# Kernel tuning notes

Measured on AMD Instinct MI355X. Metric: run time of the kernel, lower is better.

Reference implementation:

```python
import math
import jax, jax.numpy as jnp
import numpy as np

B, N1, N2 = 4, 1024, 768
DIM, H, DK = 1536, 8, 64
DV = DIM // H          # 192
NRPF = DIM // H        # 192, divisible by 6
ESM_CELL = 1280 + 256  # 1536
LN_EPS = 1e-5


def layer_norm(t, g, b):
    mu = jnp.mean(t, axis=-1, keepdims=True)
    var = jnp.mean(jnp.square(t - mu), axis=-1, keepdims=True)
    return (t - mu) * jax.lax.rsqrt(var + LN_EPS) * g + b


def positional_embed(n, feature_size):
    # Enformer-style relative positional features for distances -n+1..n-1
    distances = jnp.arange(-n + 1, n, dtype=jnp.float32)  # [2n-1]
    absd = jnp.abs(distances)[:, None]
    nb = feature_size // 6  # 3 basis fns x 2 (sym + signed)
    seq_len = float(n)
    # exponential
    max_range = math.log(seq_len) / math.log(2.0)
    half_life = 2.0 ** jnp.linspace(3.0, max_range, nb)
    f_exp = jnp.exp(-math.log(2.0) / half_life * absd)
    # central mask
    widths = 2.0 ** jnp.arange(1, nb + 1, dtype=jnp.float32) - 1.0
    f_cm = (widths[None, :] > absd).astype(jnp.float32)
    # gamma pdf
    stddev = seq_len / (2.0 * nb)
    start_mean = seq_len / nb
    mean = jnp.linspace(start_mean, seq_len, nb)
    conc = (mean / stddev) ** 2
    rate = mean / stddev ** 2
    log_p = jax.scipy.special.xlogy(conc - 1.0, absd) - rate * absd
    log_norm = jax.scipy.special.gammaln(conc) - conc * jnp.log(rate)
    prob = jnp.exp(log_p - log_norm) + 1e-8
    f_gam = prob / jnp.max(prob, axis=-1, keepdims=True)
    emb = jnp.concatenate([f_exp, f_cm, f_gam], axis=-1)
    return jnp.concatenate([emb, jnp.sign(distances)[:, None] * emb], axis=-1)  # [2n-1, feature_size]


def relative_shift(x):
    # x: [b, h, t1, 2n-1] -> [b, h, t1, n]
    b, h, t1, _ = x.shape
    x = jnp.pad(x, ((0, 0), (0, 0), (0, 0), (1, 0)))
    t2 = x.shape[-1]  # 2n
    x = x.reshape(b, h, t2, t1)[:, :, 1:, :].reshape(b, h, t1, t2 - 1)
    return x[..., : (t2 + 1) // 2]


def ffn(t, g, b, w1, b1, w2, b2):
    h = layer_norm(t, g, b)
    h = jax.nn.relu(h @ w1 + b1)
    return h @ w2 + b2


def setup_inputs() -> dict:
    key = jax.random.key(0)
    ks = jax.random.split(key, 20)
    s = 0.02
    d = {
        'x': jax.random.normal(ks[0], (B, N1, DIM), jnp.float32),
        'y0': jax.random.normal(ks[1], (B, N2, ESM_CELL), jnp.float32),
        'res_w': jax.random.normal(ks[2], (ESM_CELL, DIM)) * s,
        'lnx_g': jnp.ones((DIM,)), 'lnx_b': jnp.zeros((DIM,)),
        'lny_g': jnp.ones((DIM,)), 'lny_b': jnp.zeros((DIM,)),
        'wq': jax.random.normal(ks[3], (DIM, H * DK)) * s,
        'wk': jax.random.normal(ks[4], (DIM, H * DK)) * s,
        'wv1': jax.random.normal(ks[5], (DIM, H * DV)) * s,
        'wv2': jax.random.normal(ks[6], (DIM, H * DV)) * s,
        'wrel': jax.random.normal(ks[7], (NRPF, H * DK)) * s,
        'rel_pos_bias': jax.random.normal(ks[8], (1, H, 1, DK)),
        'wo1': jax.random.normal(ks[9], (H * DV, DIM)) * s, 'bo1': jnp.zeros((DIM,)),
        'wo2': jax.random.normal(ks[10], (H * DV, DIM)) * s, 'bo2': jnp.zeros((DIM,)),
        'fx_ln_g': jnp.ones((DIM,)), 'fx_ln_b': jnp.zeros((DIM,)),
        'fx_w1': jax.random.normal(ks[11], (DIM, 2 * DIM)) * s, 'fx_b1': jnp.zeros((2 * DIM,)),
        'fx_w2': jax.random.normal(ks[12], (2 * DIM, DIM)) * s, 'fx_b2': jnp.zeros((DIM,)),
        'fy_ln_g': jnp.ones((DIM,)), 'fy_ln_b': jnp.zeros((DIM,)),
        'fy_w1': jax.random.normal(ks[13], (DIM, 2 * DIM)) * s, 'fy_b1': jnp.zeros((2 * DIM,)),
        'fy_w2': jax.random.normal(ks[14], (2 * DIM, DIM)) * s, 'fy_b2': jnp.zeros((DIM,)),
    }
    return d


def reference(x, y0, res_w, lnx_g, lnx_b, lny_g, lny_b, wq, wk, wv1, wv2,
              wrel, rel_pos_bias, wo1, bo1, wo2, bo2,
              fx_ln_g, fx_ln_b, fx_w1, fx_b1, fx_w2, fx_b2,
              fy_ln_g, fy_ln_b, fy_w1, fy_b1, fy_w2, fy_b2):
    scale = DK ** -0.5
    y = y0 @ res_w                                   # res_proj (first layer)
    x1 = layer_norm(x, lnx_g, lnx_b)
    y1 = layer_norm(y, lny_g, lny_b)

    def heads(t, dh):  # [b, n, h*dh] -> [b, h, n, dh]
        return t.reshape(t.shape[0], t.shape[1], H, dh).transpose(0, 2, 1, 3)

    q = heads(x1 @ wq, DK) * scale                   # [b,h,n1,dk]
    k = heads(y1 @ wk, DK)                           # [b,h,n2,dk]
    v2 = heads(y1 @ wv2, DV)                         # [b,h,n2,dv]

    content = jnp.einsum('bhid,bhjd->bhij', q, k)    # [b,h,n1,n2]

    pos = positional_embed(N1, NRPF)                 # [2n1-1, nrpf]
    rel_q = (pos @ wrel).reshape(2 * N1 - 1, H, DK).transpose(1, 0, 2)  # [h,2n1-1,dk]
    rel_logits = jnp.einsum('bhjd,hnd->bhjn', k * scale + rel_pos_bias, rel_q)  # [b,h,n2,2n1-1]
    rel_logits = relative_shift(rel_logits)          # [b,h,n2,n1]
    logits = content + rel_logits.transpose(0, 1, 3, 2)

    attn = jax.nn.softmax(logits, axis=-1)           # [b,h,n1,n2]

    out1 = jnp.einsum('bhij,bhjd->bhid', attn, v2)   # [b,h,n1,dv]
    out1 = out1.transpose(0, 2, 1, 3).reshape(B, N1, H * DV)
    x2 = out1 @ wo1 + bo1

    # exchange branch: reuse attn^T on v1 from stream x
    v1 = heads(x1 @ wv1, DV)                         # [b,h,n1,dv]
    out2 = jnp.einsum('bhij,bhid->bhjd', attn, v1)   # [b,h,n2,dv]
    out2 = out2.transpose(0, 2, 1, 3).reshape(B, N2, H * DV)
    y2 = out2 @ wo2 + bo2

    x4 = x + x2
    x5 = x4 + ffn(x4, fx_ln_g, fx_ln_b, fx_w1, fx_b1, fx_w2, fx_b2)
    y4 = y + y2
    y5 = y4 + ffn(y4, fy_ln_g, fy_ln_b, fy_w1, fy_b1, fy_w2, fy_b2)
    return x5, y5
```

## Files before the change

### kernel.cpp

```cpp
#include <hip/hip_runtime.h>
#include <stdint.h>
#include <math.h>

typedef __attribute__((ext_vector_type(8))) short s8v;
typedef __attribute__((ext_vector_type(4))) short s4v;
typedef __attribute__((ext_vector_type(4))) float f4v;

#define DEV static __device__ __forceinline__

DEV short f2bf(float f) {
  uint32_t u = __builtin_bit_cast(uint32_t, f);
  u += 0x7FFFu + ((u >> 16) & 1u);
  return (short)(u >> 16);
}
DEV float bf2f(short s) {
  uint32_t u = ((uint32_t)(uint16_t)s) << 16;
  return __builtin_bit_cast(float, u);
}

#define GLD16(g, l) __builtin_amdgcn_global_load_lds( \
    (const __attribute__((address_space(1))) void*)(g), \
    (__attribute__((address_space(3))) void*)(l), 16, 0, 0)

__global__ __launch_bounds__(256) void gemm_bt(
    const short* __restrict__ A, const short* __restrict__ B,
    float* Cf, short* Cb,
    const float* __restrict__ bias, const float* resid,
    int M, int N, int K, int lda, int ldb, int ldc,
    long long sAo, long long sAi, long long sBo, long long sBi,
    long long sCo, long long sCi, float alpha, int relu)
{
  __shared__ __align__(16) short lA[128*32];
  __shared__ __align__(16) short lB[128*32];
  const int z = blockIdx.z, zo = z >> 3, zi = z & 7;
  const short* Ab = A + zo*sAo + zi*sAi;
  const short* Bb = B + zo*sBo + zi*sBi;
  const long long cOff = zo*sCo + zi*sCi;

  const int m0 = blockIdx.y*128, n0 = blockIdx.x*128;
  const int tid = threadIdx.x, lane = tid & 63, wv = tid >> 6;
  const int wm = (wv >> 1)*64, wn = (wv & 1)*64;
  const int fr = lane & 15, fq = lane >> 4;

  f4v acc[4][4] = {};

  const int rA0 = min(m0 + (tid >> 2), M - 1);
  const int rA1 = min(m0 + 64 + (tid >> 2), M - 1);
  const int rB0 = min(n0 + (tid >> 2), N - 1);
  const int rB1 = min(n0 + 64 + (tid >> 2), N - 1);
  const int pc = (tid & 3) * 8;
  const short* gA0 = Ab + (size_t)rA0*lda + pc;
  const short* gA1 = Ab + (size_t)rA1*lda + pc;
  const short* gB0 = Bb + (size_t)rB0*ldb + pc;
  const short* gB1 = Bb + (size_t)rB1*ldb + pc;
  short* dA0 = lA + (wv*64)*8;
  short* dA1 = lA + (256 + wv*64)*8;
  short* dB0 = lB + (wv*64)*8;
  short* dB1 = lB + (256 + wv*64)*8;

  for (int k0 = 0; k0 < K; k0 += 32) {
    GLD16(gA0 + k0, dA0);
    GLD16(gA1 + k0, dA1);
    GLD16(gB0 + k0, dB0);
    GLD16(gB1 + k0, dB1);
    __syncthreads();
    s8v af[4], bg[4];
#pragma unroll
    for (int i = 0; i < 4; i++) {
      af[i] = *(const s8v*)&lA[(wm + i*16 + fr)*32 + fq*8];
      bg[i] = *(const s8v*)&lB[(wn + i*16 + fr)*32 + fq*8];
    }
#pragma unroll
    for (int mi = 0; mi < 4; mi++)
#pragma unroll
      for (int ni = 0; ni < 4; ni++)
        acc[mi][ni] = __builtin_amdgcn_mfma_f32_16x16x32_bf16(af[mi], bg[ni], acc[mi][ni], 0, 0, 0);
    __syncthreads();
  }

#pragma unroll
  for (int mi = 0; mi < 4; mi++) {
    const int row = m0 + wm + mi*16 + fq*4;
#pragma unroll
    for (int ni = 0; ni < 4; ni++) {
      const int col = n0 + wn + ni*16 + fr;
      if (col >= N) continue;
      const float bv = bias ? bias[col] : 0.f;
#pragma unroll
      for (int r = 0; r < 4; r++) {
        if (row + r >= M) continue;
        float v = acc[mi][ni][r] * alpha + bv;
        const long long idx = cOff + (long long)(row + r)*ldc + col;
        if (resid) v += resid[idx];
        if (relu) v = fmaxf(v, 0.f);
        if (Cf) Cf[idx] = v;
        if (Cb) Cb[idx] = f2bf(v);
      }
    }
  }
}

#define ST_A(buf, ks, tt) do { const int ko = ((tt)<<6) + ((ks)<<5); \
    GLD16(gA0 + ko, ldA + ((buf)*2+(ks))*8192); \
    GLD16(gA1 + ko, ldA + ((buf)*2+(ks))*8192 + 4096); } while(0)
#define ST_B(buf, ks, tt) do { const int ko = ((tt)<<6) + ((ks)<<5); \
    GLD16(gB0 + ko, ldB + ((buf)*2+(ks))*8192); \
    GLD16(gB1 + ko, ldB + ((buf)*2+(ks))*8192 + 4096); } while(0)

#define PH256(buf, ks, mig, READB, DOWAIT, ...) do { \
    s8v av[4]; \
    const int rb = ((buf)*2+(ks))*8192; \
    _Pragma("unroll") for (int q2 = 0; q2 < 4; q2++) av[q2] = *(const s8v*)&smem[rb + aoff[(mig)*4+q2]]; \
    if (READB) { _Pragma("unroll") for (int q2 = 0; q2 < 4; q2++) bv[q2] = *(const s8v*)&smem[32768 + rb + boff[q2]]; } \
    __VA_ARGS__; \
    if (DOWAIT == 1) asm volatile("s_waitcnt vmcnt(6)" ::: "memory"); \
    if (DOWAIT == 2) asm volatile("s_waitcnt vmcnt(0)" ::: "memory"); \
    __builtin_amdgcn_s_barrier(); \
    asm volatile("s_waitcnt lgkmcnt(0)" ::: "memory"); \
    __builtin_amdgcn_s_setprio(1); \
    _Pragma("unroll") for (int q2 = 0; q2 < 4; q2++) \
      _Pragma("unroll") for (int u2 = 0; u2 < 4; u2++) \
        acc[(mig)*4+q2][u2] = __builtin_amdgcn_mfma_f32_16x16x32_bf16(av[q2], bv[u2], acc[(mig)*4+q2][u2], 0, 0, 0); \
    __builtin_amdgcn_s_setprio(0); \
  } while(0)

__global__ __launch_bounds__(512, 2) void gemm256(
    const short* __restrict__ A0p, const short* __restrict__ B0p,
    float* C0f, short* C0b, const float* __restrict__ bias0, const float* res0,
    int nb0, int nbm0, int N0, float al0,
    const short* __restrict__ A1p, const short* __restrict__ B1p,
    float* C1f, short* C1b, const float* __restrict__ bias1, const float* res1,
    int nb01, int nbm1, int N1, float al1,
    const short* __restrict__ A2p, const short* __restrict__ B2p,
    float* C2f, short* C2b, const float* __restrict__ bias2, const float* res2,
    int nbm2, int N2, float al2,
    int K, int relu)
{
  __shared__ __align__(16) short smem[65536];
  const int total = gridDim.x;
  int bid = blockIdx.x;
  if ((total & 7) == 0) bid = (bid & 7)*(total >> 3) + (bid >> 3);
  const short* A; const short* B; float* Cf; short* Cb; const float* bias; const float* resid;
  int tile, nbm, N; float alpha;
  if (bid < nb0)       { A = A0p; B = B0p; Cf = C0f; Cb = C0b; bias = bias0; resid = res0;
                         tile = bid; nbm = nbm0; N = N0; alpha = al0; }
  else if (bid < nb01) { A = A1p; B = B1p; Cf = C1f; Cb = C1b; bias = bias1; resid = res1;
                         tile = bid - nb0; nbm = nbm1; N = N1; alpha = al1; }
  else                 { A = A2p; B = B2p; Cf = C2f; Cb = C2b; bias = bias2; resid = res2;
                         tile = bid - nb01; nbm = nbm2; N = N2; alpha = al2; }
  const int bm = tile % nbm, bn = tile / nbm;
  const int m0 = bm << 8, n0 = bn << 8;
  const int t = threadIdx.x, lane = t & 63, w = t >> 6;
  const int wm = w >> 2, wn = w & 3;
  const int fr = lane & 15, fq = lane >> 4;
  const int ntk = K >> 6;

  const int r0 = t >> 2, r1 = 128 + (t >> 2), gsw = t & 3;
  const int cs0 = (gsw ^ ((r0 >> 1) & 3)) << 3;
  const int cs1 = (gsw ^ ((r1 >> 1) & 3)) << 3;
  const short* gA0 = A + (size_t)(m0 + r0)*K + cs0;
  const short* gA1 = A + (size_t)(m0 + r1)*K + cs1;
  const short* gB0 = B + (size_t)(n0 + r0)*K + cs0;
  const short* gB1 = B + (size_t)(n0 + r1)*K + cs1;
  short* const ldA = smem + w*512;
  short* const ldB = smem + 32768 + w*512;

  int aoff[8], boff[4];
#pragma unroll
  for (int mi = 0; mi < 8; mi++) { const int r = wm*128 + mi*16 + fr; aoff[mi] = r*32 + ((fq ^ ((r >> 1) & 3)) << 3); }
#pragma unroll
  for (int ni = 0; ni < 4; ni++) { const int r = wn*64 + ni*16 + fr; boff[ni] = r*32 + ((fq ^ ((r >> 1) & 3)) << 3); }

  f4v acc[8][4] = {};
  s8v bv[4];

  ST_A(0,0,0); ST_B(0,0,0); ST_A(0,1,0); ST_B(0,1,0);
  ST_B(1,0,1); ST_A(1,0,1); ST_B(1,1,1);
  asm volatile("s_waitcnt vmcnt(6)" ::: "memory");
  __builtin_amdgcn_s_barrier();
  asm volatile("" ::: "memory");

  for (int it = 0, nit = (ntk >> 1) - 1; it < nit; ++it) {
    const int t1 = 2*it + 1, t2 = 2*it + 2, t3 = 2*it + 3;
    PH256(0,0,0, 1,0, ST_A(1,1,t1));
    PH256(0,0,1, 0,0, ST_B(0,0,t2));
    PH256(0,1,0, 1,0, ST_A(0,0,t2));
    PH256(0,1,1, 0,1, ST_B(0,1,t2));
    PH256(1,0,0, 1,0, ST_A(0,1,t2));
    PH256(1,0,1, 0,0, ST_B(1,0,t3));
    PH256(1,1,0, 1,0, ST_A(1,0,t3));
    PH256(1,1,1, 0,1, ST_B(1,1,t3));
  }
  PH256(0,0,0, 1,0, ST_A(1,1,ntk-1));
  PH256(0,0,1, 0,0, );
  PH256(0,1,0, 1,0, );
  PH256(0,1,1, 0,2, );
  PH256(1,0,0, 1,0, );
  PH256(1,0,1, 0,0, );
  PH256(1,1,0, 1,0, );
  PH256(1,1,1, 0,0, );

#pragma unroll
  for (int mi = 0; mi < 8; mi++) {
    const int row = m0 + wm*128 + mi*16 + fq*4;
#pragma unroll
    for (int ni = 0; ni < 4; ni++) {
      const int col = n0 + wn*64 + ni*16 + fr;
      const float bvv = bias ? bias[col] : 0.f;
#pragma unroll
      for (int r = 0; r < 4; r++) {
        float v = acc[mi][ni][r]*alpha + bvv;
        const size_t idx = (size_t)(row + r)*N + col;
        if (resid) v += resid[idx];
        if (relu) v = fmaxf(v, 0.f);
        if (Cf) Cf[idx] = v;
        else Cb[idx] = f2bf(v);
      }
    }
  }
}

struct WTB {
  const float* src[8]; short* dst[8];
  int R[8], C[8], start[8];
  int NT;
};

__global__ __launch_bounds__(256) void wtransN(WTB b)
{
  __shared__ float t[32][33];
  const int id = blockIdx.x;
  if (id >= b.NT) return;
  int op = 0;
#pragma unroll
  for (int o = 1; o < 8; o++) if (id >= b.start[o]) op = o;
  const int loc = id - b.start[op];
  const int Cd = b.C[op], Rd = b.R[op];
  const int ncx = Cd >> 5;
  const int cx = (loc % ncx) << 5, ry = (loc / ncx) << 5;
  const float* s = b.src[op];
  short* d = b.dst[op];
  const int tx = threadIdx.x, ty = threadIdx.y;
#pragma unroll
  for (int k = 0; k < 4; k++)
    t[ty + k*8][tx] = s[(size_t)(ry + ty + k*8)*Cd + cx + tx];
  __syncthreads();
#pragma unroll
  for (int k = 0; k < 4; k++)
    d[(size_t)(cx + ty + k*8)*Rd + ry + tx] = f2bf(t[tx][ty + k*8]);
}

__global__ __launch_bounds__(256) void btrans(const short* __restrict__ src, short* __restrict__ dst,
    int ls, int ld_, long long sSo, long long sSi, long long sDo, long long sDi)
{
  __shared__ short t[32][33];
  const int z = blockIdx.z;
  const short* S = src + (z>>3)*sSo + (z&7)*sSi;
  short* D = dst + (z>>3)*sDo + (z&7)*sDi;
  const int c0 = blockIdx.x*32, r0 = blockIdx.y*32;
  const int tx = threadIdx.x, ty = threadIdx.y;
#pragma unroll
  for (int k = 0; k < 4; k++)
    t[ty + k*8][tx] = S[(size_t)(r0 + ty + k*8)*ls + c0 + tx];
  __syncthreads();
#pragma unroll
  for (int k = 0; k < 4; k++)
    D[(size_t)(c0 + ty + k*8)*ld_ + r0 + tx] = t[tx][ty + k*8];
}

__global__ __launch_bounds__(256) void conv_bf(const float* __restrict__ src,
                                               short* __restrict__ dst, long long n)
{
  const long long i = ((long long)blockIdx.x*256 + threadIdx.x)*4;
  if (i >= n) return;
  const float4 v = *(const float4*)(src + i);
  s4v o = { f2bf(v.x), f2bf(v.y), f2bf(v.z), f2bf(v.w) };
  *(s4v*)(dst + i) = o;
}

__global__ __launch_bounds__(256) void ln_k(const float* __restrict__ in,
    const float* __restrict__ gam, const float* __restrict__ bet, short* __restrict__ out)
{
  const long long row = blockIdx.x;
  const float* r = in + row*1536;
  const int tid = threadIdx.x;
  float v[6], s = 0.f, s2 = 0.f;
#pragma unroll
  for (int i = 0; i < 6; i++) { v[i] = r[tid + i*256]; s += v[i]; s2 += v[i]*v[i]; }
  for (int m = 1; m < 64; m <<= 1) { s += __shfl_xor(s, m); s2 += __shfl_xor(s2, m); }
  __shared__ float rs[4], rs2[4];
  if ((tid & 63) == 0) { rs[tid>>6] = s; rs2[tid>>6] = s2; }
  __syncthreads();
  s = rs[0]+rs[1]+rs[2]+rs[3]; s2 = rs2[0]+rs2[1]+rs2[2]+rs2[3];
  const float mu  = s * (1.f/1536.f);
  const float var = s2 * (1.f/1536.f) - mu*mu;
  const float inv = rsqrtf(var + 1e-5f);
  short* o = out + row*1536;
#pragma unroll
  for (int i = 0; i < 6; i++) { int c = tid + i*256; o[c] = f2bf((v[i]-mu)*inv*gam[c] + bet[c]); }
}

__global__ __launch_bounds__(64) void posemb(short* __restrict__ out)
{
  const int i = blockIdx.x;
  const int j = threadIdx.x;
  const float dist = (float)(i - 1023);
  const float absd = fabsf(dist);
  float fe = 0.f, fc = 0.f, prob = 0.f;
  if (j < 32) {
    const float hl = exp2f(3.f + 7.f*(float)j/31.f);
    fe = expf(-0.6931471805599453f/hl * absd);
    const float width = exp2f((float)(j+1)) - 1.f;
    fc = (width > absd) ? 1.f : 0.f;
    const float m = 32.f*(float)(j+1);
    const float conc = (m/16.f)*(m/16.f);
    const float rate = m/256.f;
    const float logp = (absd > 0.f ? (conc-1.f)*logf(absd) : -INFINITY) - rate*absd;
    const float logn = lgammaf(conc) - conc*logf(rate);
    prob = expf(logp - logn) + 1e-8f;
  }
  float mx = prob;
  for (int m = 1; m < 32; m <<= 1) mx = fmaxf(mx, __shfl_xor(mx, m));
  if (j < 32) {
    const float fg = prob / mx;
    const float sg = dist > 0.f ? 1.f : (dist < 0.f ? -1.f : 0.f);
    const size_t base = (size_t)i*192;
    out[base + j]       = f2bf(fe);
    out[base + 32 + j]  = f2bf(fc);
    out[base + 64 + j]  = f2bf(fg);
    out[base + 96 + j]  = f2bf(sg*fe);
    out[base + 128 + j] = f2bf(sg*fc);
    out[base + 160 + j] = f2bf(sg*fg);
  }
}

__global__ __launch_bounds__(256) void relbias_k(const float* __restrict__ rpb,
    const short* __restrict__ relq, float* __restrict__ T)
{
  const int n = blockIdx.x;
  const int tid = threadIdx.x;
  const int h = tid >> 5, l = tid & 31;
  const int d = l*2;
  float s = rpb[h*64+d]   * bf2f(relq[(size_t)n*512 + h*64 + d])
          + rpb[h*64+d+1] * bf2f(relq[(size_t)n*512 + h*64 + d+1]);
  for (int m = 1; m < 32; m <<= 1) s += __shfl_xor(s, m);
  if (l == 0) T[h*2047 + n] = s;
}

__global__ __launch_bounds__(256) void scores_k(
    const short* __restrict__ qb, const short* __restrict__ kb,
    const short* __restrict__ relq, const float* __restrict__ T,
    float* __restrict__ L)
{
  __shared__ __align__(16) short smem[21504];
  short* kt  = smem;
  short* qt  = smem + 4608;
  short* rqt = smem + 4608;
  float* P   = (float*)(smem + 4608);

  const int z = blockIdx.z, b = z >> 3, h = z & 7;
  const int j0 = blockIdx.x*64, i0 = blockIdx.y*64;
  const int tid = threadIdx.x, lane = tid & 63, wv = tid >> 6;
  const int fr = lane & 15, fq = lane >> 4;

  {
    const short* kg = kb + (size_t)(b*768  + j0)*512 + h*64;
    const short* qg = qb + (size_t)(b*1024 + i0)*512 + h*64;
    for (int c = tid; c < 512; c += 256) {
      const int r = c >> 3, ch = (c & 7)*8;
      *(s8v*)&kt[r*72 + ch] = *(const s8v*)&kg[(size_t)r*512 + ch];
      *(s8v*)&qt[r*72 + ch] = *(const s8v*)&qg[(size_t)r*512 + ch];
    }
  }
  __syncthreads();

  const int wi = (wv & 1)*32, wj = (wv >> 1)*32;
  f4v c2[2][2] = {};
#pragma unroll
  for (int ks = 0; ks < 2; ks++) {
    s8v aq[2], bk[2];
#pragma unroll
    for (int mi = 0; mi < 2; mi++) aq[mi] = *(const s8v*)&qt[(wi + mi*16 + fr)*72 + ks*32 + fq*8];
#pragma unroll
    for (int ni = 0; ni < 2; ni++) bk[ni] = *(const s8v*)&kt[(wj + ni*16 + fr)*72 + ks*32 + fq*8];
#pragma unroll
    for (int mi = 0; mi < 2; mi++)
#pragma unroll
      for (int ni = 0; ni < 2; ni++)
        c2[mi][ni] = __builtin_amdgcn_mfma_f32_16x16x32_bf16(aq[mi], bk[ni], c2[mi][ni], 0, 0, 0);
  }
  __syncthreads();

  const int nbase = 704 + i0 - j0;
  {
    const short* rg = relq + (size_t)nbase*512 + h*64;
    for (int c = tid; c < 1024; c += 256) {
      const int r = c >> 3, ch = (c & 7)*8;
      *(s8v*)&rqt[r*72 + ch] = *(const s8v*)&rg[(size_t)r*512 + ch];
    }
  }
  __syncthreads();

  const int wj2 = (wv & 1)*32, wn2 = (wv >> 1)*64;
  f4v pr[2][4] = {};
#pragma unroll
  for (int ks = 0; ks < 2; ks++) {
    s8v a2[2], b2[4];
#pragma unroll
    for (int mi = 0; mi < 2; mi++) a2[mi] = *(const s8v*)&kt[(wj2 + mi*16 + fr)*72 + ks*32 + fq*8];
#pragma unroll
    for (int ni = 0; ni < 4; ni++) b2[ni] = *(const s8v*)&rqt[(wn2 + ni*16 + fr)*72 + ks*32 + fq*8];
#pragma unroll
    for (int mi = 0; mi < 2; mi++)
#pragma unroll
      for (int ni = 0; ni < 4; ni++)
        pr[mi][ni] = __builtin_amdgcn_mfma_f32_16x16x32_bf16(a2[mi], b2[ni], pr[mi][ni], 0, 0, 0);
  }
  __syncthreads();

#pragma unroll
  for (int mi = 0; mi < 2; mi++)
#pragma unroll
    for (int ni = 0; ni < 4; ni++)
#pragma unroll
      for (int r = 0; r < 4; r++)
        P[(wj2 + mi*16 + fq*4 + r)*132 + wn2 + ni*16 + fr] = pr[mi][ni][r];
  __syncthreads();

  const float* Tt = T + h*2047 + nbase;
  float* Lb = L + ((size_t)z*1024 + i0)*768 + j0;
#pragma unroll
  for (int mi = 0; mi < 2; mi++)
#pragma unroll
    for (int ni = 0; ni < 2; ni++)
#pragma unroll
      for (int r = 0; r < 4; r++) {
        const int il = wi + mi*16 + fq*4 + r;
        const int jl = wj + ni*16 + fr;
        const int nl = 63 + il - jl;
        Lb[(size_t)il*768 + jl] = c2[mi][ni][r] + 0.125f*P[jl*132 + nl] + Tt[nl];
      }
}

__global__ __launch_bounds__(256) void softmax_k(const float* __restrict__ L, short* __restrict__ P)
{
  const long long row = blockIdx.x;
  const float* r = L + row*768;
  const int tid = threadIdx.x;
  float v0 = r[tid], v1 = r[tid+256], v2 = r[tid+512];
  float mx = fmaxf(v0, fmaxf(v1, v2));
  for (int m = 1; m < 64; m <<= 1) mx = fmaxf(mx, __shfl_xor(mx, m));
  __shared__ float redm[4], reds[4];
  if ((tid & 63) == 0) redm[tid>>6] = mx;
  __syncthreads();
  mx = fmaxf(fmaxf(redm[0], redm[1]), fmaxf(redm[2], redm[3]));
  v0 = __expf(v0 - mx); v1 = __expf(v1 - mx); v2 = __expf(v2 - mx);
  float s = v0 + v1 + v2;
  for (int m = 1; m < 64; m <<= 1) s += __shfl_xor(s, m);
  if ((tid & 63) == 0) reds[tid>>6] = s;
  __syncthreads();
  s = reds[0] + reds[1] + reds[2] + reds[3];
  const float inv = 1.f / s;
  short* o = P + row*768;
  o[tid] = f2bf(v0*inv); o[tid+256] = f2bf(v1*inv); o[tid+512] = f2bf(v2*inv);
}

static void gemm(hipStream_t st, const short* A, const short* B, float* Cf, short* Cb,
                 const float* bias, const float* resid,
                 int M, int N, int K, int lda, int ldb, int ldc,
                 int batches = 1,
                 long long sAo = 0, long long sAi = 0, long long sBo = 0, long long sBi = 0,
                 long long sCo = 0, long long sCi = 0, float alpha = 1.f, int relu = 0)
{
  dim3 g((N + 127)/128, (M + 127)/128, batches);
  gemm_bt<<<g, dim3(256), 0, st>>>(A, B, Cf, Cb, bias, resid, M, N, K, lda, ldb, ldc,
                                   sAo, sAi, sBo, sBi, sCo, sCi, alpha, relu);
}

static void g256_3(hipStream_t st,
    const short* A0, const short* B0, float* C0f, short* C0b, const float* bias0, const float* res0,
    int M0, int N0, float al0,
    const short* A1, const short* B1, float* C1f, short* C1b, const float* bias1, const float* res1,
    int M1, int N1, float al1,
    const short* A2, const short* B2, float* C2f, short* C2b, const float* bias2, const float* res2,
    int M2, int N2, float al2,
    int K, int relu)
{
  const int nbm0 = M0 >> 8, nb0 = nbm0*(N0 >> 8);
  const int nbm1 = M1 >> 8, nb1 = nbm1*(N1 >> 8);
  const int nbm2 = M2 >> 8, nb2 = M2 ? nbm2*(N2 >> 8) : 0;
  gemm256<<<dim3(nb0 + nb1 + nb2), dim3(512), 0, st>>>(
      A0, B0, C0f, C0b, bias0, res0, nb0, nbm0, N0, al0,
      A1, B1, C1f, C1b, bias1, res1, nb0 + nb1, nbm1, N1, al1,
      A2, B2, C2f, C2b, bias2, res2, nbm2, N2, al2, K, relu);
}

static void g256(hipStream_t st,
    const short* A0, const short* B0, float* C0f, short* C0b, const float* bias0, const float* res0,
    int M0, int N0, float al0,
    const short* A1, const short* B1, float* C1f, short* C1b, const float* bias1, const float* res1,
    int M1, int N1, float al1,
    int K, int relu)
{
  g256_3(st, A0, B0, C0f, C0b, bias0, res0, M0, N0, al0,
         A1, B1, C1f, C1b, bias1, res1, M1, N1, al1,
         nullptr, nullptr, nullptr, nullptr, nullptr, nullptr, 0, 256, 1.f, K, relu);
}

extern "C" void kernel_launch(void* const* d_in, const int* in_sizes, int n_in,
                              void* d_out, int out_size, void* d_ws, size_t ws_size,
                              hipStream_t stream)
{
  (void)in_sizes; (void)n_in; (void)out_size; (void)ws_size;
  const float* x     = (const float*)d_in[0];
  const float* y0    = (const float*)d_in[1];
  const float* lnxg  = (const float*)d_in[3];
  const float* lnxb  = (const float*)d_in[4];
  const float* lnyg  = (const float*)d_in[5];
  const float* lnyb  = (const float*)d_in[6];
  const float* rpb   = (const float*)d_in[12];
  const float* bo1   = (const float*)d_in[14];
  const float* bo2   = (const float*)d_in[16];
  const float* fxg   = (const float*)d_in[17];
  const float* fxbb  = (const float*)d_in[18];
  const float* fxb1  = (const float*)d_in[20];
  const float* fxb2  = (const float*)d_in[22];
  const float* fyg   = (const float*)d_in[23];
  const float* fybb  = (const float*)d_in[24];
  const float* fyb1  = (const float*)d_in[26];
  const float* fyb2  = (const float*)d_in[28];

  char* base = (char*)d_ws;
  size_t off = 0;
  auto bump = [&](size_t b) -> char* { char* p = base + off; off += (b + 255) & ~(size_t)255; return p; };

  short* W_A  = (short*)bump(4718592);
  short* W_B  = (short*)bump(1572864);
  short* W_B2 = (short*)bump(1572864);
  short* W_C  = (short*)bump(4718592);
  short* W_D  = (short*)bump(196608);
  short* W_E  = (short*)bump(9437184);
  short* W_F  = (short*)bump(9437184);

  char*  uB = bump(12582912);  short* x1 = (short*)uB;   short* out1 = (short*)uB;
  char*  uC = bump(9437184);   short* y1 = (short*)uC;   short* out2 = (short*)uC;
  char*  uD = bump(9437184);
  short* y0b = (short*)uD;
  short* qb  = (short*)uD;
  short* kbB = (short*)(uD + 4194304);
  float* Tbl   = (float*)bump(262016);
  short* posb  = (short*)bump(786048);
  short* relqb = (short*)bump(2096128);
  char*  uG = bump(12582912);  short* v1b = (short*)uG;  short* x4ln = (short*)uG;
  char*  uH = bump(9437184);   short* v2b = (short*)uH;  short* y4ln = (short*)uH;
  char*  uI = bump(100663296);
  short* wv2T   = (short*)uI;
  float* logits = (float*)uI;
  short* attnT  = (short*)uI;
  short* v1T    = (short*)(uI + 50331648);
  short* v2T    = (short*)(uI + 62914560);
  short* hx     = (short*)uI;
  short* hy     = (short*)(uI + 25165824);
  short* fy1T   = (short*)(uI + 46137344);
  short* fy2T   = (short*)(uI + 55574528);
  char*  U2 = bump(50331648);
  short* attnb = (short*)U2;
  float* y4    = (float*)U2;

  float* outx = (float*)d_out;
  float* outy = (float*)d_out + 6291456;
  float* x4  = outx;
  float* y_f = outy;

  auto addop = [&](WTB& b, int i, int idx, short* dst, int R, int C) {
    b.src[i] = (const float*)d_in[idx]; b.dst[i] = dst;
    b.R[i] = R; b.C[i] = C; b.start[i] = b.NT; b.NT += (R >> 5)*(C >> 5);
  };
  auto finwtb = [&](WTB& b, int n) {
    for (int i = n; i < 8; i++) { b.start[i] = 0x7fffffff; b.src[i] = nullptr; b.dst[i] = nullptr; b.R[i] = 32; b.C[i] = 32; }
  };

  WTB b1{}; b1.NT = 0;
  addop(b1, 0, 2,  W_A,  1536, 1536);
  addop(b1, 1, 11, W_D,  192,  512);
  addop(b1, 2, 9,  W_C,  1536, 1536);
  addop(b1, 3, 10, wv2T, 1536, 1536);
  addop(b1, 4, 7,  W_B,  1536, 512);
  addop(b1, 5, 8,  W_B2, 1536, 512);
  addop(b1, 6, 19, W_E,  1536, 3072);
  addop(b1, 7, 21, W_F,  3072, 1536);
  wtransN<<<dim3(b1.NT), dim3(32,8), 0, stream>>>(b1);

  conv_bf<<<4608, 256, 0, stream>>>(y0, y0b, 4718592LL);
  posemb<<<2047, 64, 0, stream>>>(posb);
  ln_k<<<4096, 256, 0, stream>>>(x, lnxg, lnxb, x1);
  gemm(stream, posb, W_D, nullptr, relqb, nullptr, nullptr, 2047, 512, 192, 192, 192, 512);
  relbias_k<<<2047, 256, 0, stream>>>(rpb, relqb, Tbl);
  g256(stream, y0b, W_A, y_f, nullptr, nullptr, nullptr, 3072, 1536, 1.f,
       x1, W_C, nullptr, v1b, nullptr, nullptr, 4096, 1536, 1.f, 1536, 0);
  WTB b2{}; b2.NT = 0;
  addop(b2, 0, 13, W_A, 1536, 1536);
  addop(b2, 1, 15, W_C, 1536, 1536);
  finwtb(b2, 2);
  wtransN<<<dim3(b2.NT), dim3(32,8), 0, stream>>>(b2);
  ln_k<<<3072, 256, 0, stream>>>(y_f, lnyg, lnyb, y1);
  g256_3(stream, y1, wv2T, nullptr, v2b, nullptr, nullptr, 3072, 1536, 1.f,
         x1, W_B, nullptr, qb, nullptr, nullptr, 4096, 512, 0.125f,
         y1, W_B2, nullptr, kbB, nullptr, nullptr, 3072, 512, 1.f, 1536, 0);
  scores_k<<<dim3(12,16,32), 256, 0, stream>>>(qb, kbB, relqb, Tbl, logits);
  softmax_k<<<32768, 256, 0, stream>>>(logits, attnb);
  btrans<<<dim3(24,32,32), dim3(32,8), 0, stream>>>(attnb, attnT, 768, 1024,
       8LL*786432, 786432, 8LL*786432, 786432);
  btrans<<<dim3(6,32,32), dim3(32,8), 0, stream>>>(v1b, v1T, 1536, 1024,
       1024LL*1536, 192, 8LL*196608, 196608);
  btrans<<<dim3(6,24,32), dim3(32,8), 0, stream>>>(v2b, v2T, 1536, 768,
       768LL*1536, 192, 8LL*147456, 147456);
  gemm(stream, attnb, v2T, nullptr, out1, nullptr, nullptr, 1024, 192, 768, 768, 768, 1536,
       32, 8LL*786432, 786432, 8LL*147456, 147456, 1024LL*1536, 192);
  gemm(stream, attnT, v1T, nullptr, out2, nullptr, nullptr, 768, 192, 1024, 1024, 1024, 1536,
       32, 8LL*786432, 786432, 8LL*196608, 196608, 768LL*1536, 192);
  WTB b3{}; b3.NT = 0;
  addop(b3, 0, 25, fy1T, 1536, 3072);
  addop(b3, 1, 27, fy2T, 3072, 1536);
  finwtb(b3, 2);
  wtransN<<<dim3(b3.NT), dim3(32,8), 0, stream>>>(b3);
  g256(stream, out1, W_A, x4, nullptr, bo1, x, 4096, 1536, 1.f,
       out2, W_C, y4, nullptr, bo2, y_f, 3072, 1536, 1.f, 1536, 0);
  ln_k<<<4096, 256, 0, stream>>>(x4, fxg, fxbb, x4ln);
  ln_k<<<3072, 256, 0, stream>>>(y4, fyg, fybb, y4ln);
  g256(stream, x4ln, W_E, nullptr, hx, fxb1, nullptr, 4096, 3072, 1.f,
       y4ln, fy1T, nullptr, hy, fyb1, nullptr, 3072, 3072, 1.f, 1536, 1);
  g256(stream, hx, W_F, outx, nullptr, fxb2, x4, 4096, 1536, 1.f,
       hy, fy2T, outy, nullptr, fyb2, y4, 3072, 1536, 1.f, 3072, 0);
}
```

Baseline: 697.5 us.

## Store logits in bf16 and fuse softmax with attention transpose

The scores kernel now writes logits as bf16 instead of fp32, which halves that intermediate's traffic. A new softmax kernel processes 32 rows per block, writes the normalized attention, and also writes its transpose through shared memory, so the separate btrans pass over the attention matrix is gone. Workspace aliases are rearranged (v1T/v2T reuse freed buffers) and the out2 GEMM is reordered before out1 to respect the new aliasing. Rounding logits to bf16 before softmax costs some accuracy, and the transposed store uses narrow 2-byte scattered writes.

```diff
diff --git a/kernel.cpp b/kernel.cpp
--- a/kernel.cpp
+++ b/kernel.cpp
@@ -350,7 +350,7 @@
 __global__ __launch_bounds__(256) void scores_k(
     const short* __restrict__ qb, const short* __restrict__ kb,
     const short* __restrict__ relq, const float* __restrict__ T,
-    float* __restrict__ L)
+    short* __restrict__ L)
 {
   __shared__ __align__(16) short smem[21504];
   short* kt  = smem;
@@ -428,7 +428,7 @@
   __syncthreads();
 
   const float* Tt = T + h*2047 + nbase;
-  float* Lb = L + ((size_t)z*1024 + i0)*768 + j0;
+  short* Lb = L + ((size_t)z*1024 + i0)*768 + j0;
 #pragma unroll
   for (int mi = 0; mi < 2; mi++)
 #pragma unroll
@@ -438,31 +438,60 @@
         const int il = wi + mi*16 + fq*4 + r;
         const int jl = wj + ni*16 + fr;
         const int nl = 63 + il - jl;
-        Lb[(size_t)il*768 + jl] = c2[mi][ni][r] + 0.125f*P[jl*132 + nl] + Tt[nl];
+        Lb[(size_t)il*768 + jl] = f2bf(c2[mi][ni][r] + 0.125f*P[jl*132 + nl] + Tt[nl]);
       }
 }
 
-__global__ __launch_bounds__(256) void softmax_k(const float* __restrict__ L, short* __restrict__ P)
-{
-  const long long row = blockIdx.x;
-  const float* r = L + row*768;
-  const int tid = threadIdx.x;
-  float v0 = r[tid], v1 = r[tid+256], v2 = r[tid+512];
-  float mx = fmaxf(v0, fmaxf(v1, v2));
-  for (int m = 1; m < 64; m <<= 1) mx = fmaxf(mx, __shfl_xor(mx, m));
-  __shared__ float redm[4], reds[4];
-  if ((tid & 63) == 0) redm[tid>>6] = mx;
-  __syncthreads();
-  mx = fmaxf(fmaxf(redm[0], redm[1]), fmaxf(redm[2], redm[3]));
-  v0 = __expf(v0 - mx); v1 = __expf(v1 - mx); v2 = __expf(v2 - mx);
-  float s = v0 + v1 + v2;
-  for (int m = 1; m < 64; m <<= 1) s += __shfl_xor(s, m);
-  if ((tid & 63) == 0) reds[tid>>6] = s;
-  __syncthreads();
-  s = reds[0] + reds[1] + reds[2] + reds[3];
+__global__ __launch_bounds__(256) void softmax2d(const short* __restrict__ L,
+    short* __restrict__ attnb, short* __restrict__ attnT)
+{
+  __shared__ __align__(16) short pt[32*776];
+  const int ic = blockIdx.x, z = blockIdx.y;
+  const int t = threadIdx.x, wv = t >> 6, lane = t & 63;
+  const int rl = wv*8 + (lane >> 3);
+  const int cs = (lane & 7)*96;
+  const size_t rowg = ((size_t)z*1024 + ic*32 + rl)*768;
+
+  s8v v[12];
+#pragma unroll
+  for (int k = 0; k < 12; k++) v[k] = *(const s8v*)&L[rowg + cs + k*8];
+
+  float mx = -1e30f;
+#pragma unroll
+  for (int k = 0; k < 12; k++)
+#pragma unroll
+    for (int e = 0; e < 8; e++) mx = fmaxf(mx, bf2f(v[k][e]));
+  mx = fmaxf(mx, __shfl_xor(mx, 1));
+  mx = fmaxf(mx, __shfl_xor(mx, 2));
+  mx = fmaxf(mx, __shfl_xor(mx, 4));
+
+  float s = 0.f;
+#pragma unroll
+  for (int k = 0; k < 12; k++)
+#pragma unroll
+    for (int e = 0; e < 8; e++) s += __expf(bf2f(v[k][e]) - mx);
+  s += __shfl_xor(s, 1);
+  s += __shfl_xor(s, 2);
+  s += __shfl_xor(s, 4);
   const float inv = 1.f / s;
-  short* o = P + row*768;
-  o[tid] = f2bf(v0*inv); o[tid+256] = f2bf(v1*inv); o[tid+512] = f2bf(v2*inv);
+
+  short* ab = attnb + rowg;
+#pragma unroll
+  for (int k = 0; k < 12; k++) {
+    s8v o;
+#pragma unroll
+    for (int e = 0; e < 8; e++) o[e] = f2bf(__expf(bf2f(v[k][e]) - mx) * inv);
+    *(s8v*)&ab[cs + k*8] = o;
+    *(s8v*)&pt[rl*776 + cs + k*8] = o;
+  }
+  __syncthreads();
+
+  short* aT = attnT + (size_t)z*786432 + (size_t)ic*32;
+  const int il = lane & 31, jh = lane >> 5;
+  for (int jj = 0; jj < 96; jj++) {
+    const int j = wv*192 + jj*2 + jh;
+    aT[(size_t)j*1024 + il] = pt[il*776 + j];
+  }
 }
 
 static void gemm(hipStream_t st, const short* A, const short* B, float* Cf, short* Cb,
@@ -542,27 +571,31 @@
   short* W_E  = (short*)bump(9437184);
   short* W_F  = (short*)bump(9437184);
 
-  char*  uB = bump(12582912);  short* x1 = (short*)uB;   short* out1 = (short*)uB;
-  char*  uC = bump(9437184);   short* y1 = (short*)uC;   short* out2 = (short*)uC;
+  char*  uB = bump(12582912);
+  short* x1   = (short*)uB;
+  short* v1T  = (short*)uB;
+  short* out1 = (short*)uB;
+  char*  uC = bump(9437184);
+  short* y1   = (short*)uC;
+  short* out2 = (short*)uC;
   char*  uD = bump(9437184);
   short* y0b = (short*)uD;
   short* qb  = (short*)uD;
   short* kbB = (short*)(uD + 4194304);
+  short* v2T = (short*)uD;
   float* Tbl   = (float*)bump(262016);
   short* posb  = (short*)bump(786048);
   short* relqb = (short*)bump(2096128);
   char*  uG = bump(12582912);  short* v1b = (short*)uG;  short* x4ln = (short*)uG;
   char*  uH = bump(9437184);   short* v2b = (short*)uH;  short* y4ln = (short*)uH;
   char*  uI = bump(100663296);
-  short* wv2T   = (short*)uI;
-  float* logits = (float*)uI;
-  short* attnT  = (short*)uI;
-  short* v1T    = (short*)(uI + 50331648);
-  short* v2T    = (short*)(uI + 62914560);
-  short* hx     = (short*)uI;
-  short* hy     = (short*)(uI + 25165824);
-  short* fy1T   = (short*)(uI + 46137344);
-  short* fy2T   = (short*)(uI + 55574528);
+  short* wv2T    = (short*)uI;
+  short* logits16 = (short*)uI;
+  short* attnT   = (short*)(uI + 50331648);
+  short* hx      = (short*)uI;
+  short* hy      = (short*)(uI + 25165824);
+  short* fy1T    = (short*)(uI + 46137344);
+  short* fy2T    = (short*)(uI + 55574528);
   char*  U2 = bump(50331648);
   short* attnb = (short*)U2;
   float* y4    = (float*)U2;
@@ -607,18 +640,16 @@
   g256_3(stream, y1, wv2T, nullptr, v2b, nullptr, nullptr, 3072, 1536, 1.f,
          x1, W_B, nullptr, qb, nullptr, nullptr, 4096, 512, 0.125f,
          y1, W_B2, nullptr, kbB, nullptr, nullptr, 3072, 512, 1.f, 1536, 0);
-  scores_k<<<dim3(12,16,32), 256, 0, stream>>>(qb, kbB, relqb, Tbl, logits);
-  softmax_k<<<32768, 256, 0, stream>>>(logits, attnb);
-  btrans<<<dim3(24,32,32), dim3(32,8), 0, stream>>>(attnb, attnT, 768, 1024,
-       8LL*786432, 786432, 8LL*786432, 786432);
+  scores_k<<<dim3(12,16,32), 256, 0, stream>>>(qb, kbB, relqb, Tbl, logits16);
+  softmax2d<<<dim3(32,32), 256, 0, stream>>>(logits16, attnb, attnT);
   btrans<<<dim3(6,32,32), dim3(32,8), 0, stream>>>(v1b, v1T, 1536, 1024,
        1024LL*1536, 192, 8LL*196608, 196608);
   btrans<<<dim3(6,24,32), dim3(32,8), 0, stream>>>(v2b, v2T, 1536, 768,
        768LL*1536, 192, 8LL*147456, 147456);
+  gemm(stream, attnT, v1T, nullptr, out2, nullptr, nullptr, 768, 192, 1024, 1024, 1024, 1536,
+       32, 8LL*786432, 786432, 8LL*196608, 196608, 768LL*1536, 192);
   gemm(stream, attnb, v2T, nullptr, out1, nullptr, nullptr, 1024, 192, 768, 768, 768, 1536,
        32, 8LL*786432, 786432, 8LL*147456, 147456, 1024LL*1536, 192);
-  gemm(stream, attnT, v1T, nullptr, out2, nullptr, nullptr, 768, 192, 1024, 1024, 1024, 1536,
-       32, 8LL*786432, 786432, 8LL*196608, 196608, 768LL*1536, 192);
   WTB b3{}; b3.NT = 0;
   addop(b3, 0, 25, fy1T, 1536, 3072);
   addop(b3, 1, 27, fy2T, 3072, 1536);
```

New measurement: 678.9 us. 1.03x faster.
